# Performance work log

Measured on AMD Instinct MI355X. Metric: run time of the kernel, lower is better.

The kernel has to match this reference:

```python
import jax, jax.numpy as jnp
import numpy as np

LEAKY_SLOPE = 0.01  # torch nn.LeakyReLU default

def _mlp(x, w1, b1, w2, b2):
    # MLP_Layer(num_layers=2, batch_norm=False): Linear -> ReLU -> Linear
    return jax.nn.relu(x @ w1 + b1) @ w2 + b2

def _edge_softmax(scores, dst, num_nodes):
    # softmax over incoming edges of each destination node; scores: [E, H]
    m = jax.ops.segment_max(scores, dst, num_segments=num_nodes)  # [N, H]
    e = jnp.exp(scores - m[dst])
    s = jax.ops.segment_sum(e, dst, num_segments=num_nodes)       # [N, H]
    return e / s[dst]

def setup_inputs() -> dict:
    key = jax.random.key(0)
    ks = jax.random.split(key, 10)
    N, E, H = 50000, 800000, 4
    D_H, PCA, PI, HID = 64, 64, 32, 128
    inp = {
        "h":    jax.random.normal(ks[0], (N, D_H), jnp.float32),
        "pca":  jax.random.normal(ks[1], (N, PCA), jnp.float32),
        "pimg": jax.random.normal(ks[2], (N, PI), jnp.float32),
        "pca_w1": jax.random.normal(ks[3], (2 * PCA, HID), jnp.float32) * (1.0 / np.sqrt(2 * PCA)),
        "pca_b1": jnp.zeros((HID,), jnp.float32),
        "pca_w2": jax.random.normal(ks[4], (HID, H), jnp.float32) * (1.0 / np.sqrt(HID)),
        "pca_b2": jnp.zeros((H,), jnp.float32),
        "pi_w1": jax.random.normal(ks[5], (2 * PI, HID), jnp.float32) * (1.0 / np.sqrt(2 * PI)),
        "pi_b1": jnp.zeros((HID,), jnp.float32),
        "pi_w2": jax.random.normal(ks[6], (HID, H), jnp.float32) * (1.0 / np.sqrt(HID)),
        "pi_b2": jnp.zeros((H,), jnp.float32),
        "src": jax.random.randint(ks[7], (E,), 0, N, jnp.int32),
        "dst": jax.random.randint(ks[8], (E,), 0, N, jnp.int32),
    }
    return inp

def reference(h, pca, pimg, pca_w1, pca_b1, pca_w2, pca_b2,
              pi_w1, pi_b1, pi_w2, pi_b2, src, dst):
    N = h.shape[0]

    def attend(feat, w1, b1, w2, b2):
        e_feat = jnp.concatenate([feat[src], feat[dst]], axis=1)        # [E, 2F]
        score = jax.nn.leaky_relu(_mlp(e_feat, w1, b1, w2, b2), LEAKY_SLOPE)  # [E, H]
        a = _edge_softmax(score, dst, N)                                # [E, H]
        msg = h[src][:, None, :] * a[:, :, None]                        # [E, H, D]
        return jax.ops.segment_sum(msg, dst, num_segments=N)           # [N, H, D]

    out_pca = attend(pca, pca_w1, pca_b1, pca_w2, pca_b2)
    out_pi = attend(pimg, pi_w1, pi_b1, pi_w2, pi_b2)
    return jnp.concatenate([out_pca, out_pi], axis=-1)                  # [N, H, 2D]
```

## Files before the change

kernel.cpp:

```cpp
#include <hip/hip_runtime.h>
#include <hip/hip_fp16.h>

constexpr int HID = 128;
constexpr int DH  = 64;

typedef _Float16 f16x2 __attribute__((ext_vector_type(2)));
typedef _Float16 fh8   __attribute__((ext_vector_type(8)));
typedef float    f32x4v __attribute__((ext_vector_type(4)));

__device__ __forceinline__ fh8 relu8(fh8 x) {
  fh8 z = {0, 0, 0, 0, 0, 0, 0, 0};
#if __has_builtin(__builtin_elementwise_max)
  return __builtin_elementwise_max(x, z);
#else
  fh8 r;
#pragma unroll
  for (int i = 0; i < 8; i++) r[i] = x[i] > z[i] ? x[i] : z[i];
  return r;
#endif
}

template<int F, int NB>
__launch_bounds__(256)
__global__ void uv_kernel(const float* __restrict__ feat, const float* __restrict__ w1,
                          const float* __restrict__ b1,
                          _Float16* __restrict__ u_cat, _Float16* __restrict__ v_cat,
                          int roff, int N) {
  __shared__ float sfeat[NB][F + 1];
  int nb = blockIdx.x * NB;
  for (int i = threadIdx.x; i < NB * F; i += 256) {
    int n = i / F, k = i - n * F;
    int gn = nb + n;
    sfeat[n][k] = (gn < N) ? feat[(size_t)gn * F + k] : 0.f;
  }
  __syncthreads();
  int j = threadIdx.x & 127;
  int g = threadIdx.x >> 7;
  constexpr int NPT = NB / 2;
  float ua[NPT], va[NPT];
#pragma unroll
  for (int i = 0; i < NPT; i++) { ua[i] = 0.f; va[i] = 0.f; }
  for (int k = 0; k < F; k++) {
    float wu = w1[k * HID + j];
    float wv = w1[(F + k) * HID + j];
#pragma unroll
    for (int i = 0; i < NPT; i++) {
      float f = sfeat[g * NPT + i][k];
      ua[i] = fmaf(f, wu, ua[i]);
      va[i] = fmaf(f, wv, va[i]);
    }
  }
  float b1v = b1[j];
#pragma unroll
  for (int i = 0; i < NPT; i++) {
    int gn = nb + g * NPT + i;
    if (gn < N) {
      u_cat[(size_t)gn * 256 + roff + j] = (_Float16)ua[i];
      v_cat[(size_t)gn * 256 + roff + j] = (_Float16)(va[i] + b1v);
    }
  }
}

__global__ void h16_kernel(const float* __restrict__ h, _Float16* __restrict__ h16, int total) {
  int i = (blockIdx.x * 256 + threadIdx.x) * 4;
  if (i + 3 < total) {
    float4 v = *(const float4*)(h + i);
    h16[i] = (_Float16)v.x; h16[i + 1] = (_Float16)v.y;
    h16[i + 2] = (_Float16)v.z; h16[i + 3] = (_Float16)v.w;
  } else {
    for (int q = 0; q < 4; q++) if (i + q < total) h16[i + q] = (_Float16)h[i + q];
  }
}

__global__ void count_kernel(const int* __restrict__ dst, int* __restrict__ counts, int E) {
  int e = blockIdx.x * 256 + threadIdx.x;
  if (e < E) atomicAdd(&counts[dst[e]], 1);
}

__launch_bounds__(256)
__global__ void scan1_kernel(const int* __restrict__ counts, int* __restrict__ bsums, int N) {
  int b = blockIdx.x, tid = threadIdx.x;
  int base = b * 1024 + tid * 4;
  int s = 0;
  if (base + 3 < N) {
    int4 v = *(const int4*)(counts + base);
    s = v.x + v.y + v.z + v.w;
  } else {
    for (int q = 0; q < 4; q++) { int idx = base + q; if (idx < N) s += counts[idx]; }
  }
#pragma unroll
  for (int o = 32; o >= 1; o >>= 1) s += __shfl_xor(s, o);
  __shared__ int ws[4];
  if ((tid & 63) == 0) ws[tid >> 6] = s;
  __syncthreads();
  if (tid == 0) bsums[b] = ws[0] + ws[1] + ws[2] + ws[3];
}

__launch_bounds__(1024)
__global__ void scan2_kernel(const int* __restrict__ bsums, int* __restrict__ bpre,
                             int* __restrict__ offsets, int NB, int N, int E) {
  int tid = threadIdx.x, lane = tid & 63, w = tid >> 6;
  int v = (tid < NB) ? bsums[tid] : 0;
  int incl = v;
#pragma unroll
  for (int o = 1; o < 64; o <<= 1) { int t = __shfl_up(incl, o); if (lane >= o) incl += t; }
  __shared__ int ws[16];
  if (lane == 63) ws[w] = incl;
  __syncthreads();
  int wpre = 0;
  for (int q = 0; q < w; q++) wpre += ws[q];
  if (tid < NB) bpre[tid] = wpre + incl - v;
  if (tid == 0) offsets[N] = E;
}

__launch_bounds__(256)
__global__ void scan3_kernel(const int* __restrict__ counts, const int* __restrict__ bpre,
                             int* __restrict__ offsets, int N) {
  int b = blockIdx.x, tid = threadIdx.x, lane = tid & 63, w = tid >> 6;
  int base = b * 1024 + tid * 4;
  int c[4] = {0, 0, 0, 0};
  if (base + 3 < N) {
    int4 v = *(const int4*)(counts + base);
    c[0] = v.x; c[1] = v.y; c[2] = v.z; c[3] = v.w;
  } else {
    for (int q = 0; q < 4; q++) { int idx = base + q; if (idx < N) c[q] = counts[idx]; }
  }
  int s = c[0] + c[1] + c[2] + c[3];
  int incl = s;
#pragma unroll
  for (int o = 1; o < 64; o <<= 1) { int t = __shfl_up(incl, o); if (lane >= o) incl += t; }
  int excl = incl - s;
  __shared__ int ws[4];
  if (lane == 63) ws[w] = incl;
  __syncthreads();
  int wpre = 0;
  for (int q = 0; q < w; q++) wpre += ws[q];
  int off = bpre[b] + wpre + excl;
  for (int q = 0; q < 4; q++) {
    int idx = base + q;
    if (idx < N) offsets[idx] = off;
    off += c[q];
  }
}

__global__ void fill_kernel(const int* __restrict__ src, const int* __restrict__ dst,
                            const int* __restrict__ offsets, int* __restrict__ cursor,
                            int* __restrict__ src_sorted, int* __restrict__ dst_sorted, int E) {
  int e = blockIdx.x * 256 + threadIdx.x;
  if (e < E) {
    int d = dst[e];
    int pos = offsets[d] + atomicAdd(&cursor[d], 1);
    src_sorted[pos] = src[e];
    dst_sorted[pos] = d;
  }
}

__launch_bounds__(256, 4)
__global__ void score_kernel(const _Float16* __restrict__ u_cat, const _Float16* __restrict__ v_cat,
                             const int* __restrict__ src_sorted, const int* __restrict__ dst_sorted,
                             const float* __restrict__ w2a, const float* __restrict__ w2b,
                             const float* __restrict__ b2a, const float* __restrict__ b2b,
                             _Float16* __restrict__ ek, int E) {
  int tid = threadIdx.x, lane = tid & 63, w = tid >> 6;
  int col = lane & 15, kg = lane >> 4;
  int ebase = blockIdx.x * 256 + w * 64;

  fh8 bfrag[8];
#pragma unroll
  for (int t = 0; t < 8; t++) {
#pragma unroll
    for (int j = 0; j < 8; j++) {
      int k = t * 32 + kg * 8 + j;
      float wv = 0.f;
      if (col < 4) { if (k < 128) wv = w2a[k * 4 + col]; }
      else if (col < 8) { if (k >= 128) wv = w2b[(k - 128) * 4 + (col - 4)]; }
      bfrag[t][j] = (_Float16)wv;
    }
  }

  const _Float16* up[4];
  const _Float16* vp[4];
#pragma unroll
  for (int m = 0; m < 4; m++) {
    int em = ebase + m * 16 + col;
    int ec = em < E ? em : 0;
    int s = src_sorted[ec], d = dst_sorted[ec];
    up[m] = u_cat + (size_t)s * 256 + kg * 8;
    vp[m] = v_cat + (size_t)d * 256 + kg * 8;
  }

  f32x4v acc[4];
#pragma unroll
  for (int m = 0; m < 4; m++) acc[m] = (f32x4v){0.f, 0.f, 0.f, 0.f};

#pragma unroll
  for (int t = 0; t < 8; t++) {
#pragma unroll
    for (int m = 0; m < 4; m++) {
      fh8 uu = *(const fh8*)(up[m] + t * 32);
      fh8 vv = *(const fh8*)(vp[m] + t * 32);
      fh8 af = relu8(uu + vv);
      acc[m] = __builtin_amdgcn_mfma_f32_16x16x32_f16(af, bfrag[t], acc[m], 0, 0, 0);
    }
  }

  if (col < 8) {
    float b2v = (col < 4) ? b2a[col] : b2b[col - 4];
#pragma unroll
    for (int m = 0; m < 4; m++) {
#pragma unroll
      for (int q = 0; q < 4; q++) {
        int er = ebase + m * 16 + kg * 4 + q;
        if (er < E) {
          float x = acc[m][q] + b2v;
          x = x > 0.f ? x : 0.01f * x;
          ek[(size_t)er * 8 + col] = (_Float16)__expf(x);
        }
      }
    }
  }
}

__launch_bounds__(256)
__global__ void agg_kernel(const _Float16* __restrict__ ek, const int* __restrict__ src_sorted,
                           const int* __restrict__ offsets, const _Float16* __restrict__ h16,
                           float* __restrict__ out, int N) {
  int wid = blockIdx.x * 4 + (threadIdx.x >> 6);
  int lane = threadIdx.x & 63;
  if (wid >= N) return;
  int off0 = offsets[wid], off1 = offsets[wid + 1];
  int deg = off1 - off0;
  float* op = out + (size_t)wid * 512;
  if (deg == 0) {
#pragma unroll
    for (int k = 0; k < 4; k++) { op[k * 128 + lane] = 0.f; op[k * 128 + 64 + lane] = 0.f; }
    return;
  }
  float accO[8] = {0, 0, 0, 0, 0, 0, 0, 0};
  float ssum[8] = {0, 0, 0, 0, 0, 0, 0, 0};
  int jj = 0;
  for (; jj + 2 <= deg; jj += 2) {
    size_t e0 = (size_t)(off0 + jj);
    fh8 ea = *(const fh8*)(ek + e0 * 8);
    fh8 eb = *(const fh8*)(ek + (e0 + 1) * 8);
    int sa = src_sorted[e0], sb = src_sorted[e0 + 1];
    float hva = (float)h16[(size_t)sa * DH + lane];
    float hvb = (float)h16[(size_t)sb * DH + lane];
#pragma unroll
    for (int k = 0; k < 8; k++) {
      float eav = (float)ea[k], ebv = (float)eb[k];
      accO[k] = fmaf(eav, hva, accO[k]);
      accO[k] = fmaf(ebv, hvb, accO[k]);
      ssum[k] += eav + ebv;
    }
  }
  if (jj < deg) {
    size_t e0 = (size_t)(off0 + jj);
    fh8 ea = *(const fh8*)(ek + e0 * 8);
    int sa = src_sorted[e0];
    float hva = (float)h16[(size_t)sa * DH + lane];
#pragma unroll
    for (int k = 0; k < 8; k++) {
      float eav = (float)ea[k];
      accO[k] = fmaf(eav, hva, accO[k]);
      ssum[k] += eav;
    }
  }
#pragma unroll
  for (int k = 0; k < 8; k++) {
    float rsv = 1.f / ssum[k];
    int col = k < 4 ? k * 128 + lane : (k - 4) * 128 + 64 + lane;
    op[col] = accO[k] * rsv;
  }
}

extern "C" void kernel_launch(void* const* d_in, const int* in_sizes, int n_in,
                              void* d_out, int out_size, void* d_ws, size_t ws_size,
                              hipStream_t stream) {
  const float* h      = (const float*)d_in[0];
  const float* pca    = (const float*)d_in[1];
  const float* pimg   = (const float*)d_in[2];
  const float* pca_w1 = (const float*)d_in[3];
  const float* pca_b1 = (const float*)d_in[4];
  const float* pca_w2 = (const float*)d_in[5];
  const float* pca_b2 = (const float*)d_in[6];
  const float* pi_w1  = (const float*)d_in[7];
  const float* pi_b1  = (const float*)d_in[8];
  const float* pi_w2  = (const float*)d_in[9];
  const float* pi_b2  = (const float*)d_in[10];
  const int*   src    = (const int*)d_in[11];
  const int*   dst    = (const int*)d_in[12];
  int N = in_sizes[0] / 64;
  int E = in_sizes[11];
  float* out = (float*)d_out;

  char* ws = (char*)d_ws;
  size_t o = 0;
  auto alloc = [&](size_t bytes) { void* p = ws + o; o += (bytes + 255) & ~(size_t)255; return p; };
  _Float16* u_cat = (_Float16*)alloc((size_t)N * 256 * 2);
  _Float16* v_cat = (_Float16*)alloc((size_t)N * 256 * 2);
  _Float16* h16   = (_Float16*)alloc((size_t)N * 64 * 2);
  int* counts  = (int*)alloc((size_t)N * 4);
  int* cursor  = (int*)alloc((size_t)N * 4);
  int* offsets = (int*)alloc((size_t)(N + 1) * 4);
  int* bsums   = (int*)alloc(1024 * 4);
  int* bpre    = (int*)alloc(1024 * 4);
  int* src_sorted = (int*)alloc((size_t)E * 4);
  int* dst_sorted = (int*)alloc((size_t)E * 4);
  _Float16* ekb   = (_Float16*)alloc((size_t)E * 8 * 2);

  hipMemsetAsync(counts, 0, (size_t)N * 4, stream);
  hipMemsetAsync(cursor, 0, (size_t)N * 4, stream);

  uv_kernel<64, 32><<<(N + 31) / 32, 256, 0, stream>>>(pca, pca_w1, pca_b1, u_cat, v_cat, 0, N);
  uv_kernel<32, 32><<<(N + 31) / 32, 256, 0, stream>>>(pimg, pi_w1, pi_b1, u_cat, v_cat, 128, N);
  h16_kernel<<<((N * 64) / 4 + 255) / 256, 256, 0, stream>>>(h, h16, N * 64);
  count_kernel<<<(E + 255) / 256, 256, 0, stream>>>(dst, counts, E);
  int NB = (N + 1023) / 1024;
  scan1_kernel<<<NB, 256, 0, stream>>>(counts, bsums, N);
  scan2_kernel<<<1, 1024, 0, stream>>>(bsums, bpre, offsets, NB, N, E);
  scan3_kernel<<<NB, 256, 0, stream>>>(counts, bpre, offsets, N);
  fill_kernel<<<(E + 255) / 256, 256, 0, stream>>>(src, dst, offsets, cursor, src_sorted, dst_sorted, E);
  score_kernel<<<(E + 255) / 256, 256, 0, stream>>>(u_cat, v_cat, src_sorted, dst_sorted,
                                                    pca_w2, pi_w2, pca_b2, pi_b2, ekb, E);
  agg_kernel<<<(N + 3) / 4, 256, 0, stream>>>(ekb, src_sorted, offsets, h16, out, N);
}
```

Measured before the change: 356.2 us.

## Pack edges as int2, prefetch gathers in score kernel, unroll aggregation by four

Sorted src/dst are packed into one int2 array, and the cursor is initialised by copying the offsets so fill no longer reads offsets. The score kernel stages W2 fragments in shared memory instead of keeping them in registers, and double-buffers the u/v gathers two k-steps ahead, lowering launch bounds to 3 waves. The aggregation loop processes four edges per iteration with clamped, masked loads to expose more memory-level parallelism. The risks are higher register pressure and redundant loads on low-degree nodes; agg also now reads 8-byte edge records just to get src.

```diff
diff --git a/kernel.cpp b/kernel.cpp
--- a/kernel.cpp
+++ b/kernel.cpp
@@ -144,39 +144,36 @@
 }
 
 __global__ void fill_kernel(const int* __restrict__ src, const int* __restrict__ dst,
-                            const int* __restrict__ offsets, int* __restrict__ cursor,
-                            int* __restrict__ src_sorted, int* __restrict__ dst_sorted, int E) {
+                            int* __restrict__ cursor, int2* __restrict__ edges, int E) {
   int e = blockIdx.x * 256 + threadIdx.x;
   if (e < E) {
     int d = dst[e];
-    int pos = offsets[d] + atomicAdd(&cursor[d], 1);
-    src_sorted[pos] = src[e];
-    dst_sorted[pos] = d;
-  }
-}
-
-__launch_bounds__(256, 4)
+    int pos = atomicAdd(&cursor[d], 1);
+    edges[pos] = make_int2(src[e], d);
+  }
+}
+
+__launch_bounds__(256, 3)
 __global__ void score_kernel(const _Float16* __restrict__ u_cat, const _Float16* __restrict__ v_cat,
-                             const int* __restrict__ src_sorted, const int* __restrict__ dst_sorted,
+                             const int2* __restrict__ edges,
                              const float* __restrict__ w2a, const float* __restrict__ w2b,
                              const float* __restrict__ b2a, const float* __restrict__ b2b,
                              _Float16* __restrict__ ek, int E) {
+  __shared__ _Float16 sB[8 * 64 * 8];
   int tid = threadIdx.x, lane = tid & 63, w = tid >> 6;
   int col = lane & 15, kg = lane >> 4;
+  for (int idx = tid; idx < 4096; idx += 256) {
+    int t = idx >> 9, l = (idx >> 3) & 63, j = idx & 7;
+    int bc = l & 15;
+    int k = t * 32 + ((l >> 4) << 3) + j;
+    float val = 0.f;
+    if (bc < 4) { if (k < 128) val = w2a[k * 4 + bc]; }
+    else if (bc < 8) { if (k >= 128) val = w2b[(k - 128) * 4 + (bc - 4)]; }
+    sB[idx] = (_Float16)val;
+  }
+  __syncthreads();
+
   int ebase = blockIdx.x * 256 + w * 64;
-
-  fh8 bfrag[8];
-#pragma unroll
-  for (int t = 0; t < 8; t++) {
-#pragma unroll
-    for (int j = 0; j < 8; j++) {
-      int k = t * 32 + kg * 8 + j;
-      float wv = 0.f;
-      if (col < 4) { if (k < 128) wv = w2a[k * 4 + col]; }
-      else if (col < 8) { if (k >= 128) wv = w2b[(k - 128) * 4 + (col - 4)]; }
-      bfrag[t][j] = (_Float16)wv;
-    }
-  }
 
   const _Float16* up[4];
   const _Float16* vp[4];
@@ -184,24 +181,39 @@
   for (int m = 0; m < 4; m++) {
     int em = ebase + m * 16 + col;
     int ec = em < E ? em : 0;
-    int s = src_sorted[ec], d = dst_sorted[ec];
-    up[m] = u_cat + (size_t)s * 256 + kg * 8;
-    vp[m] = v_cat + (size_t)d * 256 + kg * 8;
+    int2 sd = edges[ec];
+    up[m] = u_cat + (size_t)sd.x * 256 + kg * 8;
+    vp[m] = v_cat + (size_t)sd.y * 256 + kg * 8;
   }
 
   f32x4v acc[4];
 #pragma unroll
   for (int m = 0; m < 4; m++) acc[m] = (f32x4v){0.f, 0.f, 0.f, 0.f};
 
+  fh8 u0[4], v0[4], u1[4], v1[4];
+#pragma unroll
+  for (int m = 0; m < 4; m++) {
+    u0[m] = *(const fh8*)(up[m]);
+    v0[m] = *(const fh8*)(vp[m]);
+    u1[m] = *(const fh8*)(up[m] + 32);
+    v1[m] = *(const fh8*)(vp[m] + 32);
+  }
 #pragma unroll
   for (int t = 0; t < 8; t++) {
-#pragma unroll
-    for (int m = 0; m < 4; m++) {
-      fh8 uu = *(const fh8*)(up[m] + t * 32);
-      fh8 vv = *(const fh8*)(vp[m] + t * 32);
-      fh8 af = relu8(uu + vv);
-      acc[m] = __builtin_amdgcn_mfma_f32_16x16x32_f16(af, bfrag[t], acc[m], 0, 0, 0);
-    }
+    fh8 cu[4], cv[4];
+#pragma unroll
+    for (int m = 0; m < 4; m++) { cu[m] = u0[m]; cv[m] = v0[m]; u0[m] = u1[m]; v0[m] = v1[m]; }
+    if (t < 6) {
+#pragma unroll
+      for (int m = 0; m < 4; m++) {
+        u1[m] = *(const fh8*)(up[m] + (t + 2) * 32);
+        v1[m] = *(const fh8*)(vp[m] + (t + 2) * 32);
+      }
+    }
+    fh8 bf = *(const fh8*)(sB + ((t * 64 + lane) << 3));
+#pragma unroll
+    for (int m = 0; m < 4; m++)
+      acc[m] = __builtin_amdgcn_mfma_f32_16x16x32_f16(relu8(cu[m] + cv[m]), bf, acc[m], 0, 0, 0);
   }
 
   if (col < 8) {
@@ -222,7 +234,7 @@
 }
 
 __launch_bounds__(256)
-__global__ void agg_kernel(const _Float16* __restrict__ ek, const int* __restrict__ src_sorted,
+__global__ void agg_kernel(const _Float16* __restrict__ ek, const int2* __restrict__ edges,
                            const int* __restrict__ offsets, const _Float16* __restrict__ h16,
                            float* __restrict__ out, int N) {
   int wid = blockIdx.x * 4 + (threadIdx.x >> 6);
@@ -238,39 +250,38 @@
   }
   float accO[8] = {0, 0, 0, 0, 0, 0, 0, 0};
   float ssum[8] = {0, 0, 0, 0, 0, 0, 0, 0};
-  int jj = 0;
-  for (; jj + 2 <= deg; jj += 2) {
-    size_t e0 = (size_t)(off0 + jj);
-    fh8 ea = *(const fh8*)(ek + e0 * 8);
-    fh8 eb = *(const fh8*)(ek + (e0 + 1) * 8);
-    int sa = src_sorted[e0], sb = src_sorted[e0 + 1];
-    float hva = (float)h16[(size_t)sa * DH + lane];
-    float hvb = (float)h16[(size_t)sb * DH + lane];
+  int last = off1 - 1;
+  for (int jj = 0; jj < deg; jj += 4) {
+    int i0 = off0 + jj;
+    int i1 = min(i0 + 1, last), i2 = min(i0 + 2, last), i3 = min(i0 + 3, last);
+    bool m1 = jj + 1 < deg, m2 = jj + 2 < deg, m3 = jj + 3 < deg;
+    int s0 = edges[i0].x, s1 = edges[i1].x, s2 = edges[i2].x, s3 = edges[i3].x;
+    fh8 e0 = *(const fh8*)(ek + (size_t)i0 * 8);
+    fh8 e1 = *(const fh8*)(ek + (size_t)i1 * 8);
+    fh8 e2 = *(const fh8*)(ek + (size_t)i2 * 8);
+    fh8 e3 = *(const fh8*)(ek + (size_t)i3 * 8);
+    float hv0 = (float)h16[(size_t)s0 * DH + lane];
+    float hv1 = (float)h16[(size_t)s1 * DH + lane];
+    float hv2 = (float)h16[(size_t)s2 * DH + lane];
+    float hv3 = (float)h16[(size_t)s3 * DH + lane];
 #pragma unroll
     for (int k = 0; k < 8; k++) {
-      float eav = (float)ea[k], ebv = (float)eb[k];
-      accO[k] = fmaf(eav, hva, accO[k]);
-      accO[k] = fmaf(ebv, hvb, accO[k]);
-      ssum[k] += eav + ebv;
-    }
-  }
-  if (jj < deg) {
-    size_t e0 = (size_t)(off0 + jj);
-    fh8 ea = *(const fh8*)(ek + e0 * 8);
-    int sa = src_sorted[e0];
-    float hva = (float)h16[(size_t)sa * DH + lane];
-#pragma unroll
-    for (int k = 0; k < 8; k++) {
-      float eav = (float)ea[k];
-      accO[k] = fmaf(eav, hva, accO[k]);
-      ssum[k] += eav;
+      float e0v = (float)e0[k];
+      float e1v = m1 ? (float)e1[k] : 0.f;
+      float e2v = m2 ? (float)e2[k] : 0.f;
+      float e3v = m3 ? (float)e3[k] : 0.f;
+      accO[k] = fmaf(e0v, hv0, accO[k]);
+      accO[k] = fmaf(e1v, hv1, accO[k]);
+      accO[k] = fmaf(e2v, hv2, accO[k]);
+      accO[k] = fmaf(e3v, hv3, accO[k]);
+      ssum[k] += (e0v + e1v) + (e2v + e3v);
     }
   }
 #pragma unroll
   for (int k = 0; k < 8; k++) {
     float rsv = 1.f / ssum[k];
-    int col = k < 4 ? k * 128 + lane : (k - 4) * 128 + 64 + lane;
-    op[col] = accO[k] * rsv;
+    int colo = k < 4 ? k * 128 + lane : (k - 4) * 128 + 64 + lane;
+    op[colo] = accO[k] * rsv;
   }
 }
 
@@ -305,12 +316,10 @@
   int* offsets = (int*)alloc((size_t)(N + 1) * 4);
   int* bsums   = (int*)alloc(1024 * 4);
   int* bpre    = (int*)alloc(1024 * 4);
-  int* src_sorted = (int*)alloc((size_t)E * 4);
-  int* dst_sorted = (int*)alloc((size_t)E * 4);
-  _Float16* ekb   = (_Float16*)alloc((size_t)E * 8 * 2);
+  int2* edges  = (int2*)alloc((size_t)E * 8);
+  _Float16* ekb = (_Float16*)alloc((size_t)E * 8 * 2);
 
   hipMemsetAsync(counts, 0, (size_t)N * 4, stream);
-  hipMemsetAsync(cursor, 0, (size_t)N * 4, stream);
 
   uv_kernel<64, 32><<<(N + 31) / 32, 256, 0, stream>>>(pca, pca_w1, pca_b1, u_cat, v_cat, 0, N);
   uv_kernel<32, 32><<<(N + 31) / 32, 256, 0, stream>>>(pimg, pi_w1, pi_b1, u_cat, v_cat, 128, N);
@@ -320,8 +329,9 @@
   scan1_kernel<<<NB, 256, 0, stream>>>(counts, bsums, N);
   scan2_kernel<<<1, 1024, 0, stream>>>(bsums, bpre, offsets, NB, N, E);
   scan3_kernel<<<NB, 256, 0, stream>>>(counts, bpre, offsets, N);
-  fill_kernel<<<(E + 255) / 256, 256, 0, stream>>>(src, dst, offsets, cursor, src_sorted, dst_sorted, E);
-  score_kernel<<<(E + 255) / 256, 256, 0, stream>>>(u_cat, v_cat, src_sorted, dst_sorted,
+  hipMemcpyAsync(cursor, offsets, (size_t)N * 4, hipMemcpyDeviceToDevice, stream);
+  fill_kernel<<<(E + 255) / 256, 256, 0, stream>>>(src, dst, cursor, edges, E);
+  score_kernel<<<(E + 255) / 256, 256, 0, stream>>>(u_cat, v_cat, edges,
                                                     pca_w2, pi_w2, pca_b2, pi_b2, ekb, E);
-  agg_kernel<<<(N + 3) / 4, 256, 0, stream>>>(ekb, src_sorted, offsets, h16, out, N);
-}
+  agg_kernel<<<(N + 3) / 4, 256, 0, stream>>>(ekb, edges, offsets, h16, out, N);
+}
```

Result: faster. 336.4 us (-5.5%).
